# Kernel tuning notes

Measured on AMD Instinct MI355X. Metric: run time of the kernel, lower is better.

Reference implementation:

```python
import jax, jax.numpy as jnp
import numpy as np

C = 256
CLS_DIM = 512
GROUPS = C // 4
EPS = 1e-5


def group_norm(x, w, b, groups=GROUPS, eps=EPS):
    # x: [N, C, H, W]
    N, Cc, H, W = x.shape
    xg = x.reshape(N, groups, Cc // groups, H, W)
    mu = xg.mean(axis=(2, 3, 4), keepdims=True)
    var = xg.var(axis=(2, 3, 4), keepdims=True)
    xn = ((xg - mu) * jax.lax.rsqrt(var + eps)).reshape(N, Cc, H, W)
    return xn * w[None, :, None, None] + b[None, :, None, None]


def setup_inputs() -> dict:
    key = jax.random.key(0)
    ks = jax.random.split(key, 12)
    N, H, W = 32, 64, 64
    s = 0.02
    return {
        "X": jax.random.normal(ks[0], (N, C, H, W), jnp.float32),
        "cls": jax.random.normal(ks[1], (N, CLS_DIM), jnp.float32),
        "ln_w": 1.0 + s * jax.random.normal(ks[2], (C,), jnp.float32),
        "ln_b": s * jax.random.normal(ks[3], (C,), jnp.float32),
        "wq": jax.random.normal(ks[4], (C, CLS_DIM), jnp.float32) / np.sqrt(CLS_DIM),
        "bq": s * jax.random.normal(ks[5], (C,), jnp.float32),
        "wk": jax.random.normal(ks[6], (C, CLS_DIM), jnp.float32) / np.sqrt(CLS_DIM),
        "bk": s * jax.random.normal(ks[7], (C,), jnp.float32),
        "conv_w": jax.random.normal(ks[8], (C, C), jnp.float32) / np.sqrt(C),
        "conv_b": s * jax.random.normal(ks[9], (C,), jnp.float32),
        "gn_w": 1.0 + s * jax.random.normal(ks[10], (C,), jnp.float32),
        "gn_b": s * jax.random.normal(ks[11], (C,), jnp.float32),
    }


def reference(X, cls, ln_w, ln_b, wq, bq, wk, bk, conv_w, conv_b, gn_w, gn_b):
    res = X
    Xn = group_norm(X, ln_w, ln_b)
    # NOTE: original code swaps names: K <- Q_emb(cls), Q <- K_emb(cls)
    K = jax.nn.elu(cls @ wq.T + bq) + 1.0              # [N, C]
    Q = (jax.nn.elu(cls @ wk.T + bk) + 1.0) / jnp.sqrt(jnp.float32(C))
    # einsum 'nclw,nco->nolw' with o=1: per-pixel channel contraction with K
    s = jnp.einsum("nchw,nc->nhw", Xn, K)              # [N, H, W]
    # einsum 'nolw,nco->nclw': rank-1 outer product with Q
    X2 = s[:, None, :, :] * Q[:, :, None, None]        # [N, C, H, W]
    # 1x1 conv
    Y = jnp.einsum("nchw,oc->nohw", X2, conv_w) + conv_b[None, :, None, None]
    return group_norm(Y, gn_w, gn_b) + res
```

## Files before the change

### kernel.cpp

```cpp
#include <hip/hip_runtime.h>
#include <math.h>

#define NB 32
#define CC 256
#define CLSD 512
#define NG 64
#define HWPIX 4096
#define EPSV 1e-5f

__device__ __forceinline__ float waveReduceSum(float v) {
#pragma unroll
    for (int o = 32; o > 0; o >>= 1) v += __shfl_down(v, o, 64);
    return v;
}

__global__ void k_stats1(const float* __restrict__ X,
                         float* __restrict__ mu1, float* __restrict__ inv1) {
    int b = blockIdx.x;
    const float4* p = (const float4*)(X + (size_t)b * 16384);
    float s = 0.f, s2 = 0.f;
#pragma unroll
    for (int i = 0; i < 16; ++i) {
        float4 v = p[threadIdx.x + i * 256];
        s  += v.x + v.y + v.z + v.w;
        s2 += v.x * v.x + v.y * v.y + v.z * v.z + v.w * v.w;
    }
    __shared__ float ls[4], ls2[4];
    int lane = threadIdx.x & 63, wid = threadIdx.x >> 6;
    s = waveReduceSum(s);
    s2 = waveReduceSum(s2);
    if (lane == 0) { ls[wid] = s; ls2[wid] = s2; }
    __syncthreads();
    if (threadIdx.x == 0) {
        float S  = ls[0] + ls[1] + ls[2] + ls[3];
        float S2 = ls2[0] + ls2[1] + ls2[2] + ls2[3];
        float mu = S * (1.f / 16384.f);
        float var = S2 * (1.f / 16384.f) - mu * mu;
        mu1[b] = mu;
        inv1[b] = rsqrtf(var + EPSV);
    }
}

__global__ void k_kq(const float* __restrict__ cls,
                     const float* __restrict__ wq, const float* __restrict__ bq,
                     const float* __restrict__ wk, const float* __restrict__ bk,
                     float* __restrict__ Kb, float* __restrict__ Qb) {
    int w = blockIdx.x * 4 + (threadIdx.x >> 6);
    int lane = threadIdx.x & 63;
    int n = w >> 8, c = w & 255;
    const float* cp = cls + (size_t)n * CLSD;
    const float* qp = wq + (size_t)c * CLSD;
    const float* kp = wk + (size_t)c * CLSD;
    float aK = 0.f, aQ = 0.f;
#pragma unroll
    for (int i = 0; i < 8; ++i) {
        int kk = lane + i * 64;
        float cv = cp[kk];
        aK += cv * qp[kk];
        aQ += cv * kp[kk];
    }
    aK = waveReduceSum(aK);
    aQ = waveReduceSum(aQ);
    if (lane == 0) {
        float xk = aK + bq[c];
        float xq = aQ + bk[c];
        float Kv = (xk > 0.f ? xk : expf(xk) - 1.f) + 1.f;
        float Qv = ((xq > 0.f ? xq : expf(xq) - 1.f) + 1.f) * 0.0625f;
        Kb[w] = Kv;
        Qb[w] = Qv;
    }
}

__global__ void k_prep(const float* __restrict__ Kb, const float* __restrict__ Qb,
                       const float* __restrict__ ln_w, const float* __restrict__ ln_b,
                       const float* __restrict__ conv_w,
                       const float* __restrict__ mu1, const float* __restrict__ inv1,
                       float* __restrict__ A, float* __restrict__ B,
                       float* __restrict__ R) {
    int n = blockIdx.x, t = threadIdx.x;
    __shared__ float qs[256];
    __shared__ float red[4];
    float Kv = Kb[n * 256 + t];
    qs[t] = Qb[n * 256 + t];
    float iv = inv1[n * 64 + (t >> 2)];
    float mv = mu1[n * 64 + (t >> 2)];
    float lw = ln_w[t], lb = ln_b[t];
    A[n * 256 + t] = Kv * lw * iv;
    float termB = Kv * (lb - lw * iv * mv);
    int lane = t & 63, wid = t >> 6;
    float r = waveReduceSum(termB);
    if (lane == 0) red[wid] = r;
    __syncthreads();
    if (t == 0) B[n] = red[0] + red[1] + red[2] + red[3];
    float acc = 0.f;
    const float* cw = conv_w + (size_t)t * 256;
#pragma unroll 4
    for (int c2 = 0; c2 < 256; ++c2) acc += cw[c2] * qs[c2];
    R[n * 256 + t] = acc;
}

__global__ void k_spass(const float* __restrict__ X, const float* __restrict__ A,
                        const float* __restrict__ B, float* __restrict__ sbuf,
                        float* __restrict__ p1, float* __restrict__ p2) {
    int n = blockIdx.x >> 4, tile = blockIdx.x & 15;
    int pix = tile * 256 + threadIdx.x;
    __shared__ float as[256];
    as[threadIdx.x] = A[n * 256 + threadIdx.x];
    __syncthreads();
    const float* xp = X + (size_t)n * 256 * 4096 + pix;
    float acc = 0.f;
#pragma unroll 8
    for (int c = 0; c < 256; ++c) acc += as[c] * xp[(size_t)c * 4096];
    float s = acc + B[n];
    sbuf[n * 4096 + pix] = s;
    float r1v = waveReduceSum(s);
    float r2v = waveReduceSum(s * s);
    __shared__ float q1[4], q2[4];
    int lane = threadIdx.x & 63, wid = threadIdx.x >> 6;
    if (lane == 0) { q1[wid] = r1v; q2[wid] = r2v; }
    __syncthreads();
    if (threadIdx.x == 0) {
        p1[blockIdx.x] = q1[0] + q1[1] + q1[2] + q1[3];
        p2[blockIdx.x] = q2[0] + q2[1] + q2[2] + q2[3];
    }
}

__global__ void k_ab(const float* __restrict__ p1, const float* __restrict__ p2,
                     const float* __restrict__ R, const float* __restrict__ conv_b,
                     const float* __restrict__ gn_w, const float* __restrict__ gn_b,
                     float* __restrict__ alpha, float* __restrict__ beta) {
    int n = blockIdx.x, t = threadIdx.x;
    __shared__ float Ms1s, Ms2s;
    if (t == 0) {
        float a = 0.f, b = 0.f;
#pragma unroll
        for (int i = 0; i < 16; ++i) { a += p1[n * 16 + i]; b += p2[n * 16 + i]; }
        Ms1s = a * (1.f / 4096.f);
        Ms2s = b * (1.f / 4096.f);
    }
    __syncthreads();
    float Ms1 = Ms1s, Ms2 = Ms2s;
    int g = t >> 2;
    float mR = 0.f, mR2 = 0.f, mRb = 0.f, mb = 0.f, mb2 = 0.f;
#pragma unroll
    for (int j = 0; j < 4; ++j) {
        float r = R[n * 256 + g * 4 + j];
        float b = conv_b[g * 4 + j];
        mR += r; mR2 += r * r; mRb += r * b; mb += b; mb2 += b * b;
    }
    mR *= 0.25f; mR2 *= 0.25f; mRb *= 0.25f; mb *= 0.25f; mb2 *= 0.25f;
    float mu = Ms1 * mR + mb;
    float var = Ms2 * mR2 + 2.f * Ms1 * mRb + mb2 - mu * mu;
    float iv = rsqrtf(var + EPSV);
    float r = R[n * 256 + t];
    alpha[n * 256 + t] = r * iv * gn_w[t];
    beta[n * 256 + t] = (conv_b[t] - mu) * iv * gn_w[t] + gn_b[t];
}

__global__ void k_final(const float* __restrict__ X, const float* __restrict__ sbuf,
                        const float* __restrict__ alpha, const float* __restrict__ beta,
                        float* __restrict__ out) {
    size_t idx4 = (size_t)blockIdx.x * 256 + threadIdx.x;
    size_t e = idx4 * 4;
    int n = (int)(e >> 20);
    int rem = (int)(e & 1048575);
    int o = rem >> 12;
    int pix = rem & 4095;
    float4 x = ((const float4*)X)[idx4];
    float4 s = *(const float4*)(sbuf + n * 4096 + pix);
    float a = alpha[n * 256 + o], b = beta[n * 256 + o];
    float4 r;
    r.x = fmaf(s.x, a, b) + x.x;
    r.y = fmaf(s.y, a, b) + x.y;
    r.z = fmaf(s.z, a, b) + x.z;
    r.w = fmaf(s.w, a, b) + x.w;
    ((float4*)out)[idx4] = r;
}

extern "C" void kernel_launch(void* const* d_in, const int* in_sizes, int n_in,
                              void* d_out, int out_size, void* d_ws, size_t ws_size,
                              hipStream_t stream) {
    const float* X      = (const float*)d_in[0];
    const float* cls    = (const float*)d_in[1];
    const float* ln_w   = (const float*)d_in[2];
    const float* ln_b   = (const float*)d_in[3];
    const float* wq     = (const float*)d_in[4];
    const float* bq     = (const float*)d_in[5];
    const float* wk     = (const float*)d_in[6];
    const float* bk     = (const float*)d_in[7];
    const float* conv_w = (const float*)d_in[8];
    const float* conv_b = (const float*)d_in[9];
    const float* gn_w   = (const float*)d_in[10];
    const float* gn_b   = (const float*)d_in[11];

    float* ws = (float*)d_ws;
    float* mu1   = ws;
    float* inv1  = ws + 2048;
    float* Kb    = ws + 4096;
    float* Qb    = ws + 12288;
    float* A     = ws + 20480;
    float* B     = ws + 28672;
    float* R     = ws + 28704;
    float* p1    = ws + 36896;
    float* p2    = ws + 37408;
    float* alpha = ws + 37920;
    float* beta  = ws + 46112;
    float* sbuf  = ws + 65536;

    k_stats1<<<2048, 256, 0, stream>>>(X, mu1, inv1);
    k_kq<<<2048, 256, 0, stream>>>(cls, wq, bq, wk, bk, Kb, Qb);
    k_prep<<<32, 256, 0, stream>>>(Kb, Qb, ln_w, ln_b, conv_w, mu1, inv1, A, B, R);
    k_spass<<<512, 256, 0, stream>>>(X, A, B, sbuf, p1, p2);
    k_ab<<<32, 256, 0, stream>>>(p1, p2, R, conv_b, gn_w, gn_b, alpha, beta);
    k_final<<<32768, 256, 0, stream>>>(X, sbuf, alpha, beta, (float*)d_out);
}
```

Measured before the change: 108.7 us.

## Fuse group-norm stats with channel contraction into single pass over X

```diff
diff --git a/kernel.cpp b/kernel.cpp
--- a/kernel.cpp
+++ b/kernel.cpp
@@ -1,56 +1,28 @@
 #include <hip/hip_runtime.h>
 #include <math.h>
 
-#define NB 32
-#define CC 256
-#define CLSD 512
-#define NG 64
-#define HWPIX 4096
 #define EPSV 1e-5f
+
+typedef float f4v __attribute__((ext_vector_type(4)));
 
 __device__ __forceinline__ float waveReduceSum(float v) {
 #pragma unroll
     for (int o = 32; o > 0; o >>= 1) v += __shfl_down(v, o, 64);
     return v;
-}
-
-__global__ void k_stats1(const float* __restrict__ X,
-                         float* __restrict__ mu1, float* __restrict__ inv1) {
-    int b = blockIdx.x;
-    const float4* p = (const float4*)(X + (size_t)b * 16384);
-    float s = 0.f, s2 = 0.f;
-#pragma unroll
-    for (int i = 0; i < 16; ++i) {
-        float4 v = p[threadIdx.x + i * 256];
-        s  += v.x + v.y + v.z + v.w;
-        s2 += v.x * v.x + v.y * v.y + v.z * v.z + v.w * v.w;
-    }
-    __shared__ float ls[4], ls2[4];
-    int lane = threadIdx.x & 63, wid = threadIdx.x >> 6;
-    s = waveReduceSum(s);
-    s2 = waveReduceSum(s2);
-    if (lane == 0) { ls[wid] = s; ls2[wid] = s2; }
-    __syncthreads();
-    if (threadIdx.x == 0) {
-        float S  = ls[0] + ls[1] + ls[2] + ls[3];
-        float S2 = ls2[0] + ls2[1] + ls2[2] + ls2[3];
-        float mu = S * (1.f / 16384.f);
-        float var = S2 * (1.f / 16384.f) - mu * mu;
-        mu1[b] = mu;
-        inv1[b] = rsqrtf(var + EPSV);
-    }
 }
 
 __global__ void k_kq(const float* __restrict__ cls,
                      const float* __restrict__ wq, const float* __restrict__ bq,
                      const float* __restrict__ wk, const float* __restrict__ bk,
-                     float* __restrict__ Kb, float* __restrict__ Qb) {
+                     const float* __restrict__ ln_w,
+                     float* __restrict__ Kb, float* __restrict__ Qb,
+                     float* __restrict__ Kw) {
     int w = blockIdx.x * 4 + (threadIdx.x >> 6);
     int lane = threadIdx.x & 63;
     int n = w >> 8, c = w & 255;
-    const float* cp = cls + (size_t)n * CLSD;
-    const float* qp = wq + (size_t)c * CLSD;
-    const float* kp = wk + (size_t)c * CLSD;
+    const float* cp = cls + (size_t)n * 512;
+    const float* qp = wq + (size_t)c * 512;
+    const float* kp = wk + (size_t)c * 512;
     float aK = 0.f, aQ = 0.f;
 #pragma unroll
     for (int i = 0; i < 8; ++i) {
@@ -68,25 +40,70 @@
         float Qv = ((xq > 0.f ? xq : expf(xq) - 1.f) + 1.f) * 0.0625f;
         Kb[w] = Kv;
         Qb[w] = Qv;
-    }
-}
-
-__global__ void k_prep(const float* __restrict__ Kb, const float* __restrict__ Qb,
-                       const float* __restrict__ ln_w, const float* __restrict__ ln_b,
-                       const float* __restrict__ conv_w,
-                       const float* __restrict__ mu1, const float* __restrict__ inv1,
-                       float* __restrict__ A, float* __restrict__ B,
-                       float* __restrict__ R) {
+        Kw[w] = Kv * ln_w[c];
+    }
+}
+
+__global__ void __launch_bounds__(512) k_pass1(
+        const float* __restrict__ X, const float* __restrict__ Kw,
+        float* __restrict__ W, float* __restrict__ Sp, float* __restrict__ S2p) {
+    int n = blockIdx.x >> 4, tile = blockIdx.x & 15;
+    int wv = threadIdx.x >> 6, lane = threadIdx.x & 63;
+    __shared__ float kws[256];
+    if (threadIdx.x < 256) kws[threadIdx.x] = Kw[n * 256 + threadIdx.x];
+    __syncthreads();
+    int pix = tile * 256 + lane * 4;
+    const float* xb = X + ((size_t)n * 256 << 12) + pix;
+#pragma unroll
+    for (int go = 0; go < 8; ++go) {
+        int g = wv * 8 + go;
+        int c0 = g * 4;
+        float ax = 0.f, ay = 0.f, az = 0.f, aw = 0.f;
+        float s = 0.f, s2 = 0.f;
+#pragma unroll
+        for (int j = 0; j < 4; ++j) {
+            float4 v = *(const float4*)(xb + ((size_t)(c0 + j) << 12));
+            float kv = kws[c0 + j];
+            ax += kv * v.x; ay += kv * v.y; az += kv * v.z; aw += kv * v.w;
+            s  += v.x + v.y + v.z + v.w;
+            s2 += v.x * v.x + v.y * v.y + v.z * v.z + v.w * v.w;
+        }
+        float4 acc = {ax, ay, az, aw};
+        *(float4*)(W + ((size_t)(n * 64 + g) << 12) + pix) = acc;
+        s = waveReduceSum(s);
+        s2 = waveReduceSum(s2);
+        if (lane == 0) {
+            Sp[blockIdx.x * 64 + g] = s;
+            S2p[blockIdx.x * 64 + g] = s2;
+        }
+    }
+}
+
+__global__ void k_prep2(const float* __restrict__ Sp, const float* __restrict__ S2p,
+                        const float* __restrict__ Kb, const float* __restrict__ Qb,
+                        const float* __restrict__ ln_w, const float* __restrict__ ln_b,
+                        const float* __restrict__ conv_w,
+                        float* __restrict__ inv1, float* __restrict__ B,
+                        float* __restrict__ R) {
     int n = blockIdx.x, t = threadIdx.x;
-    __shared__ float qs[256];
-    __shared__ float red[4];
+    __shared__ float ivs[64], mus[64], qs[256], red[4];
+    qs[t] = Qb[n * 256 + t];
+    if (t < 64) {
+        float S = 0.f, S2 = 0.f;
+#pragma unroll
+        for (int tl = 0; tl < 16; ++tl) {
+            S  += Sp[(n * 16 + tl) * 64 + t];
+            S2 += S2p[(n * 16 + tl) * 64 + t];
+        }
+        float mu = S * (1.f / 16384.f);
+        float var = S2 * (1.f / 16384.f) - mu * mu;
+        float iv = rsqrtf(var + EPSV);
+        mus[t] = mu; ivs[t] = iv;
+        inv1[n * 64 + t] = iv;
+    }
+    __syncthreads();
     float Kv = Kb[n * 256 + t];
-    qs[t] = Qb[n * 256 + t];
-    float iv = inv1[n * 64 + (t >> 2)];
-    float mv = mu1[n * 64 + (t >> 2)];
-    float lw = ln_w[t], lb = ln_b[t];
-    A[n * 256 + t] = Kv * lw * iv;
-    float termB = Kv * (lb - lw * iv * mv);
+    float termB = Kv * (ln_b[t] - ln_w[t] * ivs[t >> 2] * mus[t >> 2]);
     int lane = t & 63, wid = t >> 6;
     float r = waveReduceSum(termB);
     if (lane == 0) red[wid] = r;
@@ -99,27 +116,35 @@
     R[n * 256 + t] = acc;
 }
 
-__global__ void k_spass(const float* __restrict__ X, const float* __restrict__ A,
+__global__ void k_pass3(const float* __restrict__ W, const float* __restrict__ inv1,
                         const float* __restrict__ B, float* __restrict__ sbuf,
                         float* __restrict__ p1, float* __restrict__ p2) {
-    int n = blockIdx.x >> 4, tile = blockIdx.x & 15;
-    int pix = tile * 256 + threadIdx.x;
-    __shared__ float as[256];
-    as[threadIdx.x] = A[n * 256 + threadIdx.x];
-    __syncthreads();
-    const float* xp = X + (size_t)n * 256 * 4096 + pix;
-    float acc = 0.f;
+    int n = blockIdx.x >> 2, tile = blockIdx.x & 3;
+    int t = threadIdx.x;
+    __shared__ float ivs[64];
+    __shared__ float q1[4], q2[4];
+    if (t < 64) ivs[t] = inv1[n * 64 + t];
+    __syncthreads();
+    int pix = tile * 1024 + t * 4;
+    const float* wb = W + ((size_t)n * 64 << 12) + pix;
+    float Bn = B[n];
+    float sx = Bn, sy = Bn, sz = Bn, sw = Bn;
 #pragma unroll 8
-    for (int c = 0; c < 256; ++c) acc += as[c] * xp[(size_t)c * 4096];
-    float s = acc + B[n];
-    sbuf[n * 4096 + pix] = s;
-    float r1v = waveReduceSum(s);
-    float r2v = waveReduceSum(s * s);
-    __shared__ float q1[4], q2[4];
-    int lane = threadIdx.x & 63, wid = threadIdx.x >> 6;
-    if (lane == 0) { q1[wid] = r1v; q2[wid] = r2v; }
-    __syncthreads();
-    if (threadIdx.x == 0) {
+    for (int g = 0; g < 64; ++g) {
+        float4 v = *(const float4*)(wb + ((size_t)g << 12));
+        float iv = ivs[g];
+        sx += iv * v.x; sy += iv * v.y; sz += iv * v.z; sw += iv * v.w;
+    }
+    float4 s4 = {sx, sy, sz, sw};
+    *(float4*)(sbuf + n * 4096 + pix) = s4;
+    float r1 = sx + sy + sz + sw;
+    float r2 = sx * sx + sy * sy + sz * sz + sw * sw;
+    r1 = waveReduceSum(r1);
+    r2 = waveReduceSum(r2);
+    int lane = t & 63, wid = t >> 6;
+    if (lane == 0) { q1[wid] = r1; q2[wid] = r2; }
+    __syncthreads();
+    if (t == 0) {
         p1[blockIdx.x] = q1[0] + q1[1] + q1[2] + q1[3];
         p2[blockIdx.x] = q2[0] + q2[1] + q2[2] + q2[3];
     }
@@ -134,7 +159,7 @@
     if (t == 0) {
         float a = 0.f, b = 0.f;
 #pragma unroll
-        for (int i = 0; i < 16; ++i) { a += p1[n * 16 + i]; b += p2[n * 16 + i]; }
+        for (int i = 0; i < 4; ++i) { a += p1[n * 4 + i]; b += p2[n * 4 + i]; }
         Ms1s = a * (1.f / 4096.f);
         Ms2s = b * (1.f / 4096.f);
     }
@@ -169,12 +194,12 @@
     float4 x = ((const float4*)X)[idx4];
     float4 s = *(const float4*)(sbuf + n * 4096 + pix);
     float a = alpha[n * 256 + o], b = beta[n * 256 + o];
-    float4 r;
+    f4v r;
     r.x = fmaf(s.x, a, b) + x.x;
     r.y = fmaf(s.y, a, b) + x.y;
     r.z = fmaf(s.z, a, b) + x.z;
     r.w = fmaf(s.w, a, b) + x.w;
-    ((float4*)out)[idx4] = r;
+    __builtin_nontemporal_store(r, (f4v*)out + idx4);
 }
 
 extern "C" void kernel_launch(void* const* d_in, const int* in_sizes, int n_in,
@@ -194,23 +219,25 @@
     const float* gn_b   = (const float*)d_in[11];
 
     float* ws = (float*)d_ws;
-    float* mu1   = ws;
-    float* inv1  = ws + 2048;
-    float* Kb    = ws + 4096;
-    float* Qb    = ws + 12288;
-    float* A     = ws + 20480;
-    float* B     = ws + 28672;
-    float* R     = ws + 28704;
-    float* p1    = ws + 36896;
-    float* p2    = ws + 37408;
-    float* alpha = ws + 37920;
-    float* beta  = ws + 46112;
-    float* sbuf  = ws + 65536;
-
-    k_stats1<<<2048, 256, 0, stream>>>(X, mu1, inv1);
-    k_kq<<<2048, 256, 0, stream>>>(cls, wq, bq, wk, bk, Kb, Qb);
-    k_prep<<<32, 256, 0, stream>>>(Kb, Qb, ln_w, ln_b, conv_w, mu1, inv1, A, B, R);
-    k_spass<<<512, 256, 0, stream>>>(X, A, B, sbuf, p1, p2);
+    float* Kb    = ws;
+    float* Qb    = ws + 8192;
+    float* Kw    = ws + 16384;
+    float* Sp    = ws + 24576;
+    float* S2p   = ws + 57344;
+    float* inv1  = ws + 90112;
+    float* B     = ws + 92160;
+    float* R     = ws + 92192;
+    float* p1    = ws + 100384;
+    float* p2    = ws + 100512;
+    float* alpha = ws + 100640;
+    float* beta  = ws + 108832;
+    float* sbuf  = ws + 131072;
+    float* W     = ws + 262144;
+
+    k_kq<<<2048, 256, 0, stream>>>(cls, wq, bq, wk, bk, ln_w, Kb, Qb, Kw);
+    k_pass1<<<512, 512, 0, stream>>>(X, Kw, W, Sp, S2p);
+    k_prep2<<<32, 256, 0, stream>>>(Sp, S2p, Kb, Qb, ln_w, ln_b, conv_w, inv1, B, R);
+    k_pass3<<<128, 256, 0, stream>>>(W, inv1, B, sbuf, p1, p2);
     k_ab<<<32, 256, 0, stream>>>(p1, p2, R, conv_b, gn_w, gn_b, alpha, beta);
     k_final<<<32768, 256, 0, stream>>>(X, sbuf, alpha, beta, (float*)d_out);
 }
```

After: 94.98 us. 12.6% less time.
